# Kernel optimization log

Hardware: AMD Instinct MI355X
Metric: run time of the kernel (lower is better)

Reference implementation:

```python
import jax, jax.numpy as jnp
import numpy as np

B, S, H = 2, 2048, 2048
E, K, HID = 8, 2, 4096          # num_experts, top-k, expert hidden (2*H)
NH, HD = 8, 256                  # attention heads, head_dim
MS, MD = 256, 512                # memory_size, memory_dim
RSTEPS, RD = 3, 512              # reasoning steps, reasoning_dim
SCALE = 16.0                     # sqrt(head_dim)


def setup_inputs() -> dict:
    key = jax.random.key(0)
    ks = iter(jax.random.split(key, 64))
    def w(shape, s=0.02):
        return (jax.random.normal(next(ks), shape, jnp.float32) * s)
    z = lambda *shape: jnp.zeros(shape, jnp.float32)
    inp = {
        'hidden_states': jax.random.normal(next(ks), (B, S, H), jnp.float32),
        'attention_mask': jnp.zeros((B, S), jnp.float32),  # 0 = unmasked (faithful: mask*-1e9 added)
        # MoE
        'gate_w': w((H, E)), 'gate_b': z(E),
        'moe_w1': w((E, H, HID)), 'moe_b1': z(E, HID),
        'moe_w2': w((E, HID, H)), 'moe_b2': z(E, H),
        # memory-augmented attention
        'q_w': w((H, H)), 'q_b': z(H),
        'k_w': w((H, H)), 'k_b': z(H),
        'v_w': w((H, H)), 'v_b': z(H),
        'o_w': w((H, H)), 'o_b': z(H),
        'mem_values': jax.random.normal(next(ks), (MS, MD), jnp.float32),
        'mem_proj_w': w((MD, H)), 'mem_proj_b': z(H),
        'mem_attn_w': w((H, MS)), 'mem_attn_b': z(MS),
        # hierarchical reasoning (stacked over steps)
        'rs_w1': w((RSTEPS, H, RD)), 'rs_b1': z(RSTEPS, RD),
        'rs_w2': w((RSTEPS, RD, H)), 'rs_b2': z(RSTEPS, H),
        'ln_g': jnp.ones((RSTEPS, H), jnp.float32), 'ln_b': z(RSTEPS, H),
        'hg_w1': w((RSTEPS, H, H // 4)), 'hg_b1': z(RSTEPS, H // 4),
        'hg_w2': w((RSTEPS, H // 4, 1)), 'hg_b2': z(RSTEPS, 1),
        'integ_w': w((RSTEPS * H, H)), 'integ_b': z(H),
    }
    return inp


def _layernorm(x, g, b, eps=1e-5):
    m = x.mean(-1, keepdims=True)
    v = ((x - m) ** 2).mean(-1, keepdims=True)
    return (x - m) / jnp.sqrt(v + eps) * g + b


def _forward(hidden_states, attention_mask, gate_w, gate_b, moe_w1, moe_b1, moe_w2, moe_b2,
             q_w, q_b, k_w, k_b, v_w, v_b, o_w, o_b, mem_values, mem_proj_w, mem_proj_b,
             mem_attn_w, mem_attn_b, rs_w1, rs_b1, rs_w2, rs_b2, ln_g, ln_b,
             hg_w1, hg_b1, hg_w2, hg_b2, integ_w, integ_b):
    h = hidden_states
    N = B * S
    # ---- Mixture of Experts (top-k routing, dense combine-weight formulation) ----
    x_flat = h.reshape(N, H)
    gate_probs = jax.nn.softmax(x_flat @ gate_w + gate_b, axis=-1)        # [N,E]
    topk_s, topk_i = jax.lax.top_k(gate_probs, K)                          # [N,K]
    topk_p = jax.nn.softmax(topk_s, axis=-1)                               # renormalize over top-k
    comb = jnp.zeros((N, E), x_flat.dtype).at[jnp.arange(N)[:, None], topk_i].add(topk_p)
    h1 = jax.nn.relu(jnp.einsum('nd,edh->neh', x_flat, moe_w1) + moe_b1)   # [N,E,HID]
    eo = jnp.einsum('neh,ehd->ned', h1, moe_w2) + moe_b2                   # [N,E,H]
    moe_out = jnp.einsum('ned,ne->nd', eo, comb).reshape(B, S, H)
    h = h + 0.5 * moe_out
    # ---- Memory-augmented attention ----
    q = (h @ q_w + q_b).reshape(B, S, NH, HD).transpose(0, 2, 1, 3)
    k = (h @ k_w + k_b).reshape(B, S, NH, HD).transpose(0, 2, 1, 3)
    v = (h @ v_w + v_b).reshape(B, S, NH, HD).transpose(0, 2, 1, 3)
    scores = jnp.einsum('bhqd,bhkd->bhqk', q, k) / SCALE
    scores = scores + attention_mask[:, None, None, :] * (-1e9)
    probs = jax.nn.softmax(scores, axis=-1)
    attn = jnp.einsum('bhqk,bhkd->bhqd', probs, v).transpose(0, 2, 1, 3).reshape(B, S, H)
    mem_p = jax.nn.softmax(h @ mem_attn_w + mem_attn_b, axis=-1)           # [B,S,MS]
    mem_o = (mem_p @ mem_values) @ mem_proj_w + mem_proj_b                 # [B,S,H]
    mem_out = (attn + 0.3 * mem_o) @ o_w + o_b
    h = h + mem_out
    # ---- Hierarchical reasoning ----
    cur = h
    outs = []
    for i in range(RSTEPS):
        so = jax.nn.relu(cur @ rs_w1[i] + rs_b1[i]) @ rs_w2[i] + rs_b2[i]
        so = _layernorm(so, ln_g[i], ln_b[i])
        g = jax.nn.sigmoid(jax.nn.relu(cur @ hg_w1[i] + hg_b1[i]) @ hg_w2[i] + hg_b2[i])  # [B,S,1]
        cur = cur + g * so
        outs.append(cur)
    final = jnp.concatenate(outs, axis=-1) @ integ_w + integ_b
    return h + final


def reference(hidden_states, attention_mask, gate_w, gate_b, moe_w1, moe_b1, moe_w2, moe_b2,
              q_w, q_b, k_w, k_b, v_w, v_b, o_w, o_b, mem_values, mem_proj_w, mem_proj_b,
              mem_attn_w, mem_attn_b, rs_w1, rs_b1, rs_w2, rs_b2, ln_g, ln_b,
              hg_w1, hg_b1, hg_w2, hg_b2, integ_w, integ_b):
    return _forward(hidden_states, attention_mask, gate_w, gate_b, moe_w1, moe_b1, moe_w2, moe_b2,
                    q_w, q_b, k_w, k_b, v_w, v_b, o_w, o_b, mem_values, mem_proj_w, mem_proj_b,
                    mem_attn_w, mem_attn_b, rs_w1, rs_b1, rs_w2, rs_b2, ln_g, ln_b,
                    hg_w1, hg_b1, hg_w2, hg_b2, integ_w, integ_b)
```

## Files before the change

kernel.cpp:

```cpp
#include <hip/hip_runtime.h>
#include <string.h>


typedef __attribute__((ext_vector_type(4))) float f32x4;
typedef __attribute__((ext_vector_type(8))) __bf16 bf16x8;

#define NTOK 4096
#define HDIM 2048
#define AS1 __attribute__((address_space(1)))
#define AS3 __attribute__((address_space(3)))

__device__ __forceinline__ unsigned short f2bf(float f) {
  unsigned u = __float_as_uint(f);
  unsigned r = (u + 0x7fffu + ((u >> 16) & 1u)) >> 16;
  return (unsigned short)r;
}
__device__ __forceinline__ float bf2f(unsigned short u) {
  return __uint_as_float(((unsigned)u) << 16);
}
__device__ __forceinline__ void unpack8(uint4 r, float* v) {
  v[0]=bf2f((unsigned short)(r.x&0xffff)); v[1]=bf2f((unsigned short)(r.x>>16));
  v[2]=bf2f((unsigned short)(r.y&0xffff)); v[3]=bf2f((unsigned short)(r.y>>16));
  v[4]=bf2f((unsigned short)(r.z&0xffff)); v[5]=bf2f((unsigned short)(r.z>>16));
  v[6]=bf2f((unsigned short)(r.w&0xffff)); v[7]=bf2f((unsigned short)(r.w>>16));
}
__device__ __forceinline__ uint4 pack8(const float* v) {
  uint4 r;
  r.x = (unsigned)f2bf(v[0]) | ((unsigned)f2bf(v[1])<<16);
  r.y = (unsigned)f2bf(v[2]) | ((unsigned)f2bf(v[3])<<16);
  r.z = (unsigned)f2bf(v[4]) | ((unsigned)f2bf(v[5])<<16);
  r.w = (unsigned)f2bf(v[6]) | ((unsigned)f2bf(v[7])<<16);
  return r;
}

__global__ void k_tconv(const float* __restrict__ in, unsigned short* __restrict__ out,
                        int R, int C, long inB, long outB) {
  __shared__ float tl[32][33];
  const int z = blockIdx.z;
  const float* ip = in + (long)z * inB;
  unsigned short* op = out + (long)z * outB;
  const int tx = threadIdx.x & 31, ty = threadIdx.x >> 5;
  const int c0 = blockIdx.x * 32, r0 = blockIdx.y * 32;
#pragma unroll
  for (int i = 0; i < 4; i++)
    tl[ty + i*8][tx] = ip[(long)(r0 + ty + i*8) * C + c0 + tx];
  __syncthreads();
#pragma unroll
  for (int i = 0; i < 4; i++)
    op[(long)(c0 + ty + i*8) * R + r0 + tx] = f2bf(tl[tx][ty + i*8]);
}

__global__ void k_tconv4(const float* __restrict__ i0, const float* __restrict__ i1,
                         const float* __restrict__ i2, const float* __restrict__ i3,
                         unsigned short* __restrict__ out) {
  __shared__ float tl[32][33];
  const int z = blockIdx.z;
  const float* ip = (z == 0) ? i0 : (z == 1) ? i1 : (z == 2) ? i2 : i3;
  unsigned short* op = out + ((z < 3) ? (size_t)z * 2048 * 2048 : (size_t)6400 * 2048);
  const int tx = threadIdx.x & 31, ty = threadIdx.x >> 5;
  const int c0 = blockIdx.x * 32, r0 = blockIdx.y * 32;
#pragma unroll
  for (int i = 0; i < 4; i++)
    tl[ty + i*8][tx] = ip[(long)(r0 + ty + i*8) * 2048 + c0 + tx];
  __syncthreads();
#pragma unroll
  for (int i = 0; i < 4; i++)
    op[(long)(c0 + ty + i*8) * 2048 + r0 + tx] = f2bf(tl[tx][ty + i*8]);
}

__global__ void k_tvact(const unsigned short* __restrict__ qkv, unsigned short* __restrict__ vT) {
  __shared__ unsigned short tl[32][33];
  const int z = blockIdx.z, b = z >> 3, hh = z & 7;
  const unsigned short* ip = qkv + (long)b * 2048 * 6400 + 4096 + hh * 256;
  unsigned short* op = vT + (long)z * 256 * 2048;
  const int tx = threadIdx.x & 31, ty = threadIdx.x >> 5;
  const int d0 = blockIdx.x * 32, s0 = blockIdx.y * 32;
#pragma unroll
  for (int i = 0; i < 4; i++)
    tl[ty + i*8][tx] = ip[(long)(s0 + ty + i*8) * 6400 + d0 + tx];
  __syncthreads();
#pragma unroll
  for (int i = 0; i < 4; i++)
    op[(long)(d0 + ty + i*8) * 2048 + s0 + tx] = tl[tx][ty + i*8];
}

__global__ void k_misc(const float* __restrict__ mask, float* __restrict__ mv,
                       const float* __restrict__ qb, const float* __restrict__ kb,
                       const float* __restrict__ vb, const float* __restrict__ mb,
                       float* __restrict__ qkvb,
                       const float* __restrict__ rsb1, const float* __restrict__ hgb1,
                       float* __restrict__ rhb, int* __restrict__ meta) {
  const int b = blockIdx.x, t = threadIdx.x;
  if (b < 16) {
    int i = b * 256 + t; mv[i] = -1e9f * mask[i];
  } else if (b < 41) {
    int i = (b - 16) * 256 + t;
    if (i < 6400)
      qkvb[i] = (i < 2048) ? qb[i] : (i < 4096) ? kb[i - 2048]
              : (i < 6144) ? vb[i - 4096] : mb[i - 6144];
  } else if (b < 47) {
    int i = (b - 41) * 256 + t;
    int s = i >> 9, c = i & 511;
    rhb[s * 1024 + c] = rsb1[i]; rhb[s * 1024 + 512 + c] = hgb1[i];
  } else {
    if (t < 8) meta[t] = 0;
  }
}

__global__ void k_gate(const float* __restrict__ x, const float* __restrict__ gw,
                       const float* __restrict__ gb, int* __restrict__ meta,
                       int* __restrict__ e0a, int* __restrict__ e1a,
                       float* __restrict__ w0a, float* __restrict__ w1a,
                       unsigned short* __restrict__ xb) {
  const int wv = threadIdx.x >> 6, ln = threadIdx.x & 63;
  const int n = blockIdx.x * 4 + wv;
  const float* xr = x + (long)n * HDIM;
  unsigned short* xo = xb + (long)n * HDIM;
  float s[8] = {0,0,0,0,0,0,0,0};
  for (int k = ln; k < HDIM; k += 64) {
    float xv = xr[k];
    xo[k] = f2bf(xv);
    const float* g = gw + (long)k * 8;
#pragma unroll
    for (int e = 0; e < 8; e++) s[e] += xv * g[e];
  }
#pragma unroll
  for (int e = 0; e < 8; e++)
    for (int d = 32; d; d >>= 1) s[e] += __shfl_xor(s[e], d);
  if (ln == 0) {
    float mx = -1e30f;
#pragma unroll
    for (int e = 0; e < 8; e++) { s[e] += gb[e]; mx = fmaxf(mx, s[e]); }
    float p[8], sum = 0.f;
#pragma unroll
    for (int e = 0; e < 8; e++) { p[e] = expf(s[e] - mx); sum += p[e]; }
    float inv = 1.f / sum;
#pragma unroll
    for (int e = 0; e < 8; e++) p[e] *= inv;
    int e0 = 0;
    for (int e = 1; e < 8; e++) if (p[e] > p[e0]) e0 = e;
    int e1 = (e0 == 0) ? 1 : 0;
    for (int e = 0; e < 8; e++) if (e != e0 && p[e] > p[e1]) e1 = e;
    float q = expf(p[e1] - p[e0]);
    float w0 = 1.f / (1.f + q), w1 = q / (1.f + q);
    e0a[n] = e0; e1a[n] = e1; w0a[n] = w0; w1a[n] = w1;
    atomicAdd(&meta[e0], 1); atomicAdd(&meta[e1], 1);
  }
}

__global__ void k_buildmap(int* meta) {
  if (threadIdx.x == 0 && blockIdx.x == 0) {
    int cum = 0, nT = 0;
    for (int e = 0; e < 8; e++) {
      int c = meta[e];
      meta[16 + e] = cum; meta[24 + e] = cum + c; meta[8 + e] = 0;
      int t = (c + 127) >> 7;
      for (int i = 0; i < t; i++) { meta[33 + nT] = e; meta[129 + nT] = cum + i * 128; nT++; }
      cum += c;
    }
    meta[32] = nT;
  }
}

__global__ void k_scatter(int* __restrict__ meta, const int* __restrict__ e0a,
                          const int* __restrict__ e1a, int* __restrict__ s0a,
                          int* __restrict__ s1a, int* __restrict__ srcTok) {
  const int n = blockIdx.x * 256 + threadIdx.x;
  if (n < NTOK) {
    int e0 = e0a[n], e1 = e1a[n];
    int s0 = meta[16 + e0] + atomicAdd(&meta[8 + e0], 1);
    int s1 = meta[16 + e1] + atomicAdd(&meta[8 + e1], 1);
    s0a[n] = s0; s1a[n] = s1; srcTok[s0] = n; srcTok[s1] = n;
  }
}

__global__ void k_combine(const float* __restrict__ h, const unsigned short* __restrict__ eo,
                          const int* __restrict__ s0a, const int* __restrict__ s1a,
                          const float* __restrict__ w0a, const float* __restrict__ w1a,
                          unsigned short* __restrict__ h2b) {
  const int n = blockIdx.x, c = threadIdx.x * 8;
  const float w0 = w0a[n], w1 = w1a[n];
  uint4 a = *(const uint4*)(eo + (long)s0a[n] * HDIM + c);
  uint4 b = *(const uint4*)(eo + (long)s1a[n] * HDIM + c);
  float va[8], vb[8]; unpack8(a, va); unpack8(b, vb);
  const float* hr = h + (long)n * HDIM + c;
  float o[8];
#pragma unroll
  for (int j = 0; j < 8; j++) o[j] = hr[j] + 0.5f * (w0 * va[j] + w1 * vb[j]);
  *(uint4*)(h2b + (long)n * HDIM + c) = pack8(o);
}

__global__ void k_softmax256(const unsigned short* __restrict__ in, long ld,
                             unsigned short* __restrict__ out) {
  const int wv = threadIdx.x >> 6, ln = threadIdx.x & 63;
  const long r = (long)blockIdx.x * 4 + wv;
  uint2 raw = ((const uint2*)(in + r * ld))[ln];
  float v[4];
  v[0]=bf2f((unsigned short)(raw.x&0xffff)); v[1]=bf2f((unsigned short)(raw.x>>16));
  v[2]=bf2f((unsigned short)(raw.y&0xffff)); v[3]=bf2f((unsigned short)(raw.y>>16));
  float m = fmaxf(fmaxf(v[0], v[1]), fmaxf(v[2], v[3]));
  for (int d = 32; d; d >>= 1) m = fmaxf(m, __shfl_xor(m, d));
  float s = 0.f;
#pragma unroll
  for (int j = 0; j < 4; j++) { v[j] = expf(v[j] - m); s += v[j]; }
  for (int d = 32; d; d >>= 1) s += __shfl_xor(s, d);
  const float inv = 1.f / s;
  union { unsigned short u[4]; uint2 d2; } p;
#pragma unroll
  for (int j = 0; j < 4; j++) p.u[j] = f2bf(v[j] * inv);
  ((uint2*)(out + r * 256))[ln] = p.d2;
}

__global__ void k_gdot(const unsigned short* __restrict__ g1, long ld, const float* __restrict__ w,
                       const float* __restrict__ bb, float* __restrict__ gv) {
  const int wv = threadIdx.x >> 6, ln = threadIdx.x & 63;
  const int n = blockIdx.x * 4 + wv;
  uint4 raw = *(const uint4*)(g1 + (long)n * ld + ln * 8);
  float v[8]; unpack8(raw, v);
  const float4 wa = ((const float4*)w)[ln * 2];
  const float4 wb = ((const float4*)w)[ln * 2 + 1];
  float s = v[0]*wa.x + v[1]*wa.y + v[2]*wa.z + v[3]*wa.w
          + v[4]*wb.x + v[5]*wb.y + v[6]*wb.z + v[7]*wb.w;
  for (int d = 32; d; d >>= 1) s += __shfl_xor(s, d);
  if (ln == 0) gv[n] = 1.f / (1.f + expf(-(s + bb[0])));
}

__global__ void k_lnupdate(const unsigned short* __restrict__ so,
                           const unsigned short* __restrict__ curIn,
                           const float* __restrict__ gv, const float* __restrict__ lng,
                           const float* __restrict__ lnb,
                           unsigned short* __restrict__ curbOut,
                           unsigned short* __restrict__ outs, int step) {
  const int n = blockIdx.x, t = threadIdx.x, wv = t >> 6, ln = t & 63, c = t * 8;
  uint4 raw = *(const uint4*)(so + (long)n * 2048 + c);
  float x[8]; unpack8(raw, x);
  float s1 = 0.f, s2 = 0.f;
#pragma unroll
  for (int j = 0; j < 8; j++) { s1 += x[j]; s2 += x[j] * x[j]; }
  for (int d = 32; d; d >>= 1) { s1 += __shfl_xor(s1, d); s2 += __shfl_xor(s2, d); }
  __shared__ float a1[4], a2[4];
  if (ln == 0) { a1[wv] = s1; a2[wv] = s2; }
  __syncthreads();
  s1 = a1[0] + a1[1] + a1[2] + a1[3];
  s2 = a2[0] + a2[1] + a2[2] + a2[3];
  const float mean = s1 * (1.f / 2048.f);
  const float var = s2 * (1.f / 2048.f) - mean * mean;
  const float rstd = rsqrtf(var + 1e-5f);
  const float g = gv[n];
  uint4 ci = *(const uint4*)(curIn + (long)n * 2048 + c);
  float cv[8]; unpack8(ci, cv);
  float o[8];
#pragma unroll
  for (int j = 0; j < 8; j++) {
    float l = (x[j] - mean) * rstd * lng[c + j] + lnb[c + j];
    o[j] = cv[j] + g * l;
  }
  const uint4 pk = pack8(o);
  *(uint4*)(curbOut + (long)n * 2048 + c) = pk;
  *(uint4*)(outs + (long)n * 6144 + (long)step * 2048 + c) = pk;
}

struct GArgs {
  const unsigned short* A; long lda, aSO, aSI;
  const unsigned short* Bt; long ldb, bSO, bSI;
  int M, N, K;
  const float* adv; long advSO, advSI;
  float alpha, rscale;
  const float* rF; long ldrF, rfSO, rfSI;
  const unsigned short* rB; long ldrB, rbSO, rbSI;
  float* oF; long ldoF, ofSO, ofSI;
  unsigned short* oB; long ldoB, obSO, obSI;
  const int* meta;
  const int* srcTok;
};

template <int MOE, int RELU, int RESID, int OUTF, int OUTB>
__global__ __launch_bounds__(512) void gemm_bt(GArgs g) {
  __shared__ unsigned short lds[2 * 16384];
  const int t = threadIdx.x, wv = t >> 6, ln = t & 63, ln15 = ln & 15;
  const int lr8 = ln >> 3;
  const int lsl = (ln & 7) ^ lr8;
  const int bz = blockIdx.z;
  int row0, rowMax;
  const unsigned short *A, *Bt;
  long advO = 0, rFO = 0, rBO = 0, oFO = 0, oBO = 0;
  if constexpr (MOE) {
    const int ty = blockIdx.y;
    if (ty >= g.meta[32]) return;
    const int e = g.meta[33 + ty];
    row0 = g.meta[129 + ty]; rowMax = g.meta[24 + e];
    A = g.A; Bt = g.Bt + (long)e * g.bSO;
    advO = (long)e * g.advSO;
  } else {
    row0 = blockIdx.y << 7; rowMax = g.M;
    const long bo = (long)(bz >> 3), bi = (long)(bz & 7);
    A = g.A + bo * g.aSO + bi * g.aSI;
    Bt = g.Bt + bo * g.bSO + bi * g.bSI;
    advO = bo * g.advSO + bi * g.advSI;
    rFO = bo * g.rfSO + bi * g.rfSI;
    rBO = bo * g.rbSO + bi * g.rbSI;
    oFO = bo * g.ofSO + bi * g.ofSI;
    oBO = bo * g.obSO + bi * g.obSI;
  }
  const int col0 = blockIdx.x << 7;
  const long lda = g.lda, ldb = g.ldb;
  const int wm = (wv >> 2) << 6;
  const int wc = (wv & 3) << 5;

  int grow0, grow1;
  {
    int r0i = row0 + (wv << 4) + lr8;
    int r1i = r0i + 8;
    if constexpr (MOE) {
      r0i = (r0i < rowMax) ? r0i : (rowMax - 1);
      r1i = (r1i < rowMax) ? r1i : (rowMax - 1);
    }
    if constexpr (MOE == 2) { grow0 = g.srcTok[r0i]; grow1 = g.srcTok[r1i]; }
    else { grow0 = r0i; grow1 = r1i; }
  }

  auto STAGE = [&](int kt, unsigned base) {
    const long kk = ((long)kt << 6) + (lsl << 3);
    {
      const int rb = (wv << 4);
      __builtin_amdgcn_global_load_lds(
          (const AS1 void*)(A + (long)grow0 * lda + kk),
          (AS3 void*)(lds + base + (rb << 6)), 16, 0, 0);
      __builtin_amdgcn_global_load_lds(
          (const AS1 void*)(A + (long)grow1 * lda + kk),
          (AS3 void*)(lds + base + ((rb + 8) << 6)), 16, 0, 0);
    }
#pragma unroll
    for (int l = 0; l < 2; ++l) {
      const int rb = (wv << 4) + (l << 3);
      __builtin_amdgcn_global_load_lds(
          (const AS1 void*)(Bt + (long)(col0 + rb + lr8) * ldb + kk),
          (AS3 void*)(lds + base + 8192 + (rb << 6)), 16, 0, 0);
    }
  };

  const f32x4 fz = {0.f, 0.f, 0.f, 0.f};
  f32x4 acc[4][2];
#pragma unroll
  for (int i = 0; i < 4; i++)
#pragma unroll
    for (int j = 0; j < 2; j++) acc[i][j] = fz;

  const int nt = g.K >> 6;

  STAGE(0, 0);
  asm volatile("s_waitcnt vmcnt(0)" ::: "memory");
  __builtin_amdgcn_s_barrier();

  for (int kt = 0; kt < nt; ++kt) {
    const unsigned aB = (kt & 1) ? 16384u : 0u;
    const unsigned nB = aB ^ 16384u;
    if (kt + 1 < nt) STAGE(kt + 1, nB);
#pragma unroll
    for (int ks = 0; ks < 2; ++ks) {
      const int kb = (ks << 2) + (ln >> 4);
      bf16x8 bg[2];
#pragma unroll
      for (int j = 0; j < 2; ++j) {
        const int r = wc + (j << 4) + ln15;
        bg[j] = *(const bf16x8*)(lds + aB + 8192 + (r << 6) + ((kb ^ (r & 7)) << 3));
      }
      __builtin_amdgcn_s_setprio(1);
#pragma unroll
      for (int i = 0; i < 4; ++i) {
        const int r = wm + (i << 4) + ln15;
        bf16x8 a = *(const bf16x8*)(lds + aB + (r << 6) + ((kb ^ (r & 7)) << 3));
#pragma unroll
        for (int j = 0; j < 2; ++j)
          acc[i][j] = __builtin_amdgcn_mfma_f32_16x16x32_bf16(a, bg[j], acc[i][j], 0, 0, 0);
      }
      __builtin_amdgcn_s_setprio(0);
    }
    asm volatile("s_waitcnt vmcnt(0)" ::: "memory");
    __builtin_amdgcn_s_barrier();
  }

#pragma unroll
  for (int i = 0; i < 4; i++) {
#pragma unroll
    for (int j = 0; j < 2; j++) {
      const int cc = col0 + wc + (j << 4) + ln15;
      const float av = g.adv ? g.adv[advO + cc] : 0.f;
#pragma unroll
      for (int r = 0; r < 4; r++) {
        const int rr = row0 + wm + (i << 4) + ((ln >> 4) << 2) + r;
        if (rr < rowMax) {
          float v = g.alpha * acc[i][j][r] + av;
          if constexpr (RELU) v = fmaxf(v, 0.f);
          if constexpr (RESID == 1) v = g.rF[rFO + (long)rr * g.ldrF + cc] + g.rscale * v;
          if constexpr (RESID == 2) v = bf2f(g.rB[rBO + (long)rr * g.ldrB + cc]) + g.rscale * v;
          if constexpr (OUTF) g.oF[oFO + (long)rr * g.ldoF + cc] = v;
          if constexpr (OUTB) g.oB[oBO + (long)rr * g.ldoB + cc] = f2bf(v);
        }
      }
    }
  }
}

__global__ __launch_bounds__(512) void k_fa(const unsigned short* __restrict__ qkvm,
                                            const unsigned short* __restrict__ Vt,
                                            const float* __restrict__ msk,
                                            unsigned short* __restrict__ O) {
  __shared__ unsigned short sm[34816];
  __shared__ float msk_s[2048];
  __shared__ float m_run[64], l_run[64], fac[64], mnv[64], tsm[128], tss[128];
  const int t = threadIdx.x, wv = t >> 6, ln = t & 63, ln15 = ln & 15;
  const int rt = blockIdx.x, bh = blockIdx.y;
  const int b = bh >> 3, hh = bh & 7;
  const int q0 = rt << 6;
  const unsigned short* Bq = qkvm + (long)b * 2048 * 6400;

#pragma unroll
  for (int l = 0; l < 4; ++l) {
    const int li = l * 512 + t;
    const int p = li >> 9, r = (li >> 3) & 63, s = li & 7;
    __builtin_amdgcn_global_load_lds(
        (const AS1 void*)(Bq + (long)(q0 + r) * 6400 + hh * 256 + p * 64 + ((s ^ (r & 7)) << 3)),
        (AS3 void*)(sm + li * 8), 16, 0, 0);
  }
#pragma unroll
  for (int l = 0; l < 4; ++l) {
    const int i = l * 512 + t;
    msk_s[i] = msk[b * 2048 + i];
  }
  if (t < 64) { m_run[t] = -3.0e38f; l_run[t] = 0.f; }

  auto STAGEKV = [&](int kt) {
#pragma unroll
    for (int l = 0; l < 2; ++l) {
      const int li = l * 512 + t;
      const int p = li >> 8, r = (li >> 3) & 31, s = li & 7;
      __builtin_amdgcn_global_load_lds(
          (const AS1 void*)(Bq + (long)(kt * 32 + r) * 6400 + 2048 + hh * 256 + p * 64 + ((s ^ (r & 7)) << 3)),
          (AS3 void*)(sm + 16384 + li * 8), 16, 0, 0);
    }
#pragma unroll
    for (int l = 0; l < 2; ++l) {
      const int li = l * 512 + t;
      const int r = li >> 2, s = li & 3;
      __builtin_amdgcn_global_load_lds(
          (const AS1 void*)(Vt + (long)bh * 524288 + (long)r * 2048 + kt * 32 + ((s ^ ((r >> 1) & 3)) << 3)),
          (AS3 void*)(sm + 24576 + li * 8), 16, 0, 0);
    }
  };
  STAGEKV(0);
  asm volatile("s_waitcnt vmcnt(0)" ::: "memory");
  __syncthreads();

  const int rw = wv >> 1, cw = wv & 1;
  const int wc = wv << 5;
  const int rowbase = (rw << 4) + ((ln >> 4) << 2);
  const f32x4 fz = {0.f, 0.f, 0.f, 0.f};
  f32x4 acc[4][2];
#pragma unroll
  for (int i = 0; i < 4; i++)
#pragma unroll
    for (int j = 0; j < 2; j++) acc[i][j] = fz;

  for (int kt = 0; kt < 64; ++kt) {
    f32x4 sAcc = fz;
#pragma unroll
    for (int ks = 0; ks < 8; ++ks) {
      const int kp = ks >> 1;
      const int kb = ((ks & 1) << 2) + (ln >> 4);
      const int ra = (rw << 4) + ln15;
      bf16x8 a = *(const bf16x8*)(sm + kp * 4096 + (ra << 6) + ((kb ^ (ra & 7)) << 3));
      const int rb = (cw << 4) + ln15;
      bf16x8 bb = *(const bf16x8*)(sm + 16384 + kp * 2048 + (rb << 6) + ((kb ^ (rb & 7)) << 3));
      sAcc = __builtin_amdgcn_mfma_f32_16x16x32_bf16(a, bb, sAcc, 0, 0, 0);
    }
    float sv[4];
    const float mk = msk_s[(kt << 5) + (cw << 4) + ln15];
#pragma unroll
    for (int r = 0; r < 4; ++r) {
      sv[r] = sAcc[r] * 0.0625f + mk;
      float mr = sv[r];
#pragma unroll
      for (int d = 1; d < 16; d <<= 1) mr = fmaxf(mr, __shfl_xor(mr, d));
      if (ln15 == 0) tsm[((rowbase + r) << 1) + cw] = mr;
    }
    __syncthreads();
    if (t < 64) {
      if (kt > 0) l_run[t] = l_run[t] * fac[t] + tss[t << 1] + tss[(t << 1) + 1];
      const float mt = fmaxf(tsm[t << 1], tsm[(t << 1) + 1]);
      const float mn = fmaxf(m_run[t], mt);
      fac[t] = expf(m_run[t] - mn);
      mnv[t] = mn; m_run[t] = mn;
    }
    __syncthreads();
#pragma unroll
    for (int r = 0; r < 4; ++r) {
      const int row = rowbase + r;
      const float p = expf(sv[r] - mnv[row]);
      const int col = (cw << 4) + ln15;
      sm[32768 + (row << 5) + (((col >> 3) ^ ((row >> 1) & 3)) << 3) + (col & 7)] = f2bf(p);
      float sr = p;
#pragma unroll
      for (int d = 1; d < 16; d <<= 1) sr += __shfl_xor(sr, d);
      if (ln15 == 0) tss[(row << 1) + cw] = sr;
    }
#pragma unroll
    for (int i = 0; i < 4; ++i) {
      const int rw2 = (i << 4) + ((ln >> 4) << 2);
#pragma unroll
      for (int r = 0; r < 4; ++r) {
        const float fv = fac[rw2 + r];
        acc[i][0][r] *= fv; acc[i][1][r] *= fv;
      }
    }
    __syncthreads();
    const int kb2 = ln >> 4;
#pragma unroll
    for (int i = 0; i < 4; ++i) {
      const int ra = (i << 4) + ln15;
      bf16x8 a = *(const bf16x8*)(sm + 32768 + (ra << 5) + ((kb2 ^ ((ra >> 1) & 3)) << 3));
#pragma unroll
      for (int j = 0; j < 2; ++j) {
        const int rv = wc + (j << 4) + ln15;
        bf16x8 bv = *(const bf16x8*)(sm + 24576 + (rv << 5) + ((kb2 ^ ((rv >> 1) & 3)) << 3));
        acc[i][j] = __builtin_amdgcn_mfma_f32_16x16x32_bf16(a, bv, acc[i][j], 0, 0, 0);
      }
    }
    __syncthreads();
    if (kt + 1 < 64) STAGEKV(kt + 1);
    asm volatile("s_waitcnt vmcnt(0)" ::: "memory");
    __syncthreads();
  }
  if (t < 64) {
    const float l = l_run[t] * fac[t] + tss[t << 1] + tss[(t << 1) + 1];
    fac[t] = 1.f / l;
  }
  __syncthreads();
  unsigned short* Ob = O + (long)b * 2048 * 2048 + hh * 256;
#pragma unroll
  for (int i = 0; i < 4; ++i) {
#pragma unroll
    for (int j = 0; j < 2; ++j) {
      const int cc = wc + (j << 4) + ln15;
#pragma unroll
      for (int r = 0; r < 4; ++r) {
        const int row = (i << 4) + ((ln >> 4) << 2) + r;
        Ob[(long)(q0 + row) * 2048 + cc] = f2bf(acc[i][j][r] * fac[row]);
      }
    }
  }
}

static constexpr size_t O_W1T = 0;
static constexpr size_t O_W2T = O_W1T + (size_t)8 * 4096 * 2048 * 2;
static constexpr size_t O_QT  = O_W2T + (size_t)8 * 4096 * 2048 * 2;
static constexpr size_t O_OT  = O_QT + (size_t)6400 * 2048 * 2;
static constexpr size_t O_MPT = O_QT + (size_t)8448 * 2048 * 2;
static constexpr size_t O_MVT = O_MPT + (size_t)2048 * 512 * 2;
static constexpr size_t O_RH1 = O_MVT + (size_t)512 * 256 * 2;
static constexpr size_t O_RS2 = O_RH1 + (size_t)3 * 1024 * 2048 * 2;
static constexpr size_t O_IGT = O_RS2 + (size_t)3 * 2048 * 512 * 2;
static constexpr size_t O_META= O_IGT + (size_t)2048 * 6144 * 2;
static constexpr size_t O_E0  = O_META + 4096;
static constexpr size_t O_E1  = O_E0 + 16384;
static constexpr size_t O_W0  = O_E1 + 16384;
static constexpr size_t O_W1  = O_W0 + 16384;
static constexpr size_t O_S0  = O_W1 + 16384;
static constexpr size_t O_S1  = O_S0 + 16384;
static constexpr size_t O_SRC = O_S1 + 16384;
static constexpr size_t O_MSK = O_SRC + 32768;
static constexpr size_t O_GV  = O_MSK + 16384;
static constexpr size_t O_QKVB= O_GV + 16384;
static constexpr size_t O_RHB = O_QKVB + 6400 * 4;
static constexpr size_t O_H2B = O_RHB + 3072 * 4;
static constexpr size_t O_H3B = O_H2B + (size_t)4096 * 2048 * 2;
static constexpr size_t O_ATT = O_H3B + (size_t)4096 * 2048 * 2;
static constexpr size_t O_AO2 = O_ATT + (size_t)4096 * 2048 * 2;
static constexpr size_t O_MPB = O_AO2 + (size_t)4096 * 2048 * 2;
static constexpr size_t O_MPV = O_MPB + (size_t)4096 * 256 * 2;
static constexpr size_t O_AR  = O_MPV + (size_t)4096 * 512 * 2;
static constexpr size_t O_XB = O_AR;
static constexpr size_t O_H1 = O_XB + (size_t)4096 * 2048 * 2 + (size_t)8192 * 2048 * 2;
static constexpr size_t O_EO = O_H1 + (size_t)8192 * 4096 * 2;
static constexpr size_t O_QB = O_XB + (size_t)4096 * 2048 * 2;
static constexpr size_t O_VT = O_QB + (size_t)4096 * 6400 * 2;
static constexpr size_t O_T1 = O_QB;
static constexpr size_t O_SOB= O_T1 + (size_t)4096 * 1024 * 2;
static constexpr size_t O_CRB= O_SOB + (size_t)4096 * 2048 * 2;
static constexpr size_t O_OUS= O_CRB + (size_t)4096 * 2048 * 2;

extern "C" void kernel_launch(void* const* d_in, const int* in_sizes, int n_in,
                              void* d_out, int out_size, void* d_ws, size_t ws_size,
                              hipStream_t stream) {
  (void)in_sizes; (void)n_in; (void)out_size; (void)ws_size;
  const float* h        = (const float*)d_in[0];
  const float* mask     = (const float*)d_in[1];
  const float* gate_w   = (const float*)d_in[2];
  const float* gate_b   = (const float*)d_in[3];
  const float* moe_w1   = (const float*)d_in[4];
  const float* moe_b1   = (const float*)d_in[5];
  const float* moe_w2   = (const float*)d_in[6];
  const float* moe_b2   = (const float*)d_in[7];
  const float* q_w      = (const float*)d_in[8];
  const float* q_b      = (const float*)d_in[9];
  const float* k_w      = (const float*)d_in[10];
  const float* k_b      = (const float*)d_in[11];
  const float* v_w      = (const float*)d_in[12];
  const float* v_b      = (const float*)d_in[13];
  const float* o_w      = (const float*)d_in[14];
  const float* o_b      = (const float*)d_in[15];
  const float* mem_vals = (const float*)d_in[16];
  const float* mproj_w  = (const float*)d_in[17];
  const float* mproj_b  = (const float*)d_in[18];
  const float* mattn_w  = (const float*)d_in[19];
  const float* mattn_b  = (const float*)d_in[20];
  const float* rs_w1    = (const float*)d_in[21];
  const float* rs_b1    = (const float*)d_in[22];
  const float* rs_w2    = (const float*)d_in[23];
  const float* rs_b2    = (const float*)d_in[24];
  const float* ln_g     = (const float*)d_in[25];
  const float* ln_b     = (const float*)d_in[26];
  const float* hg_w1    = (const float*)d_in[27];
  const float* hg_b1    = (const float*)d_in[28];
  const float* hg_w2    = (const float*)d_in[29];
  const float* hg_b2    = (const float*)d_in[30];
  const float* integ_w  = (const float*)d_in[31];
  const float* integ_b  = (const float*)d_in[32];

  char* ws = (char*)d_ws;
  auto U = [&](size_t o) { return (unsigned short*)(ws + o); };
  auto F = [&](size_t o) { return (float*)(ws + o); };
  auto I = [&](size_t o) { return (int*)(ws + o); };

  k_tconv<<<dim3(128, 64, 8), 256, 0, stream>>>(moe_w1, U(O_W1T), 2048, 4096, 8388608, 8388608);
  k_tconv<<<dim3(64, 128, 8), 256, 0, stream>>>(moe_w2, U(O_W2T), 4096, 2048, 8388608, 8388608);
  k_tconv4<<<dim3(64, 64, 4), 256, 0, stream>>>(q_w, k_w, v_w, o_w, U(O_QT));
  k_tconv<<<dim3(8, 64, 1), 256, 0, stream>>>(mattn_w, U(O_QT) + (size_t)6144 * 2048, 2048, 256, 0, 0);
  k_tconv<<<dim3(64, 16, 1), 256, 0, stream>>>(mproj_w, U(O_MPT), 512, 2048, 0, 0);
  k_tconv<<<dim3(16, 8, 1), 256, 0, stream>>>(mem_vals, U(O_MVT), 256, 512, 0, 0);
  k_tconv<<<dim3(16, 64, 3), 256, 0, stream>>>(rs_w1, U(O_RH1), 2048, 512, 2048 * 512, 1024 * 2048);
  k_tconv<<<dim3(16, 64, 3), 256, 0, stream>>>(hg_w1, U(O_RH1) + (size_t)512 * 2048, 2048, 512,
                                               2048 * 512, 1024 * 2048);
  k_tconv<<<dim3(64, 16, 3), 256, 0, stream>>>(rs_w2, U(O_RS2), 512, 2048, 512 * 2048, 512 * 2048);
  k_tconv<<<dim3(64, 192, 1), 256, 0, stream>>>(integ_w, U(O_IGT), 6144, 2048, 0, 0);
  k_misc<<<48, 256, 0, stream>>>(mask, F(O_MSK), q_b, k_b, v_b, mattn_b, F(O_QKVB),
                                 rs_b1, hg_b1, F(O_RHB), I(O_META));

  k_gate<<<1024, 256, 0, stream>>>(h, gate_w, gate_b, I(O_META), I(O_E0), I(O_E1),
                                   F(O_W0), F(O_W1), U(O_XB));
  k_buildmap<<<1, 1, 0, stream>>>(I(O_META));
  k_scatter<<<16, 256, 0, stream>>>(I(O_META), I(O_E0), I(O_E1), I(O_S0), I(O_S1), I(O_SRC));

  GArgs z0; memset(&z0, 0, sizeof(z0)); z0.alpha = 1.f; z0.rscale = 1.f;
  {
    GArgs g = z0;
    g.A = U(O_XB); g.lda = 2048;
    g.Bt = U(O_W1T); g.ldb = 2048; g.bSO = (long)4096 * 2048;
    g.N = 4096; g.K = 2048;
    g.adv = moe_b1; g.advSO = 4096;
    g.oB = U(O_H1); g.ldoB = 4096;
    g.meta = I(O_META); g.srcTok = I(O_SRC);
    gemm_bt<2, 1, 0, 0, 1><<<dim3(32, 72, 1), 512, 0, stream>>>(g);
  }
  {
    GArgs g = z0;
    g.A = U(O_H1); g.lda = 4096;
    g.Bt = U(O_W2T); g.ldb = 4096; g.bSO = (long)2048 * 4096;
    g.N = 2048; g.K = 4096;
    g.adv = moe_b2; g.advSO = 2048;
    g.oB = U(O_EO); g.ldoB = 2048;
    g.meta = I(O_META);
    gemm_bt<1, 0, 0, 0, 1><<<dim3(16, 72, 1), 512, 0, stream>>>(g);
  }
  k_combine<<<4096, 256, 0, stream>>>(h, U(O_EO), I(O_S0), I(O_S1), F(O_W0), F(O_W1), U(O_H2B));

  {
    GArgs g = z0;
    g.A = U(O_H2B); g.lda = 2048; g.M = 4096; g.N = 6400; g.K = 2048;
    g.Bt = U(O_QT); g.ldb = 2048;
    g.adv = F(O_QKVB);
    g.oB = U(O_QB); g.ldoB = 6400;
    gemm_bt<0, 0, 0, 0, 1><<<dim3(50, 32, 1), 512, 0, stream>>>(g);
  }
  k_tvact<<<dim3(8, 64, 16), 256, 0, stream>>>(U(O_QB), U(O_VT));
  k_fa<<<dim3(32, 16, 1), 512, 0, stream>>>(U(O_QB), U(O_VT), F(O_MSK), U(O_ATT));
  k_softmax256<<<1024, 256, 0, stream>>>(U(O_QB) + 6144, 6400, U(O_MPB));
  {
    GArgs g = z0;
    g.A = U(O_MPB); g.lda = 256; g.Bt = U(O_MVT); g.ldb = 256;
    g.M = 4096; g.N = 512; g.K = 256;
    g.oB = U(O_MPV); g.ldoB = 512;
    gemm_bt<0, 0, 0, 0, 1><<<dim3(4, 32, 1), 512, 0, stream>>>(g);
  }
  {
    GArgs g = z0;
    g.A = U(O_MPV); g.lda = 512; g.Bt = U(O_MPT); g.ldb = 512;
    g.M = 4096; g.N = 2048; g.K = 512;
    g.adv = mproj_b;
    g.rB = U(O_ATT); g.ldrB = 2048; g.rscale = 0.3f;
    g.oB = U(O_AO2); g.ldoB = 2048;
    gemm_bt<0, 0, 2, 0, 1><<<dim3(16, 32, 1), 512, 0, stream>>>(g);
  }
  {
    GArgs g = z0;
    g.A = U(O_AO2); g.lda = 2048; g.Bt = U(O_OT); g.ldb = 2048;
    g.M = 4096; g.N = 2048; g.K = 2048;
    g.adv = o_b;
    g.rB = U(O_H2B); g.ldrB = 2048; g.rscale = 1.f;
    g.oB = U(O_H3B); g.ldoB = 2048;
    gemm_bt<0, 0, 2, 0, 1><<<dim3(16, 32, 1), 512, 0, stream>>>(g);
  }

  for (int i = 0; i < 3; i++) {
    const unsigned short* curb = (i == 0) ? U(O_H3B) : U(O_CRB);
    {
      GArgs g = z0;
      g.A = curb; g.lda = 2048;
      g.Bt = U(O_RH1) + (size_t)i * 1024 * 2048; g.ldb = 2048;
      g.M = 4096; g.N = 1024; g.K = 2048;
      g.adv = F(O_RHB) + i * 1024;
      g.oB = U(O_T1); g.ldoB = 1024;
      gemm_bt<0, 1, 0, 0, 1><<<dim3(8, 32, 1), 512, 0, stream>>>(g);
    }
    {
      GArgs g = z0;
      g.A = U(O_T1); g.lda = 1024;
      g.Bt = U(O_RS2) + (size_t)i * 2048 * 512; g.ldb = 512;
      g.M = 4096; g.N = 2048; g.K = 512;
      g.adv = rs_b2 + i * 2048;
      g.oB = U(O_SOB); g.ldoB = 2048;
      gemm_bt<0, 0, 0, 0, 1><<<dim3(16, 32, 1), 512, 0, stream>>>(g);
    }
    k_gdot<<<1024, 256, 0, stream>>>(U(O_T1) + 512, 1024, hg_w2 + i * 512, hg_b2 + i, F(O_GV));
    k_lnupdate<<<4096, 256, 0, stream>>>(U(O_SOB), curb, F(O_GV), ln_g + i * 2048,
                                         ln_b + i * 2048, U(O_CRB), U(O_OUS), i);
  }
  {
    GArgs g = z0;
    g.A = U(O_OUS); g.lda = 6144; g.Bt = U(O_IGT); g.ldb = 6144;
    g.M = 4096; g.N = 2048; g.K = 6144;
    g.adv = integ_b;
    g.rB = U(O_H3B); g.ldrB = 2048; g.rscale = 1.f;
    g.oF = (float*)d_out; g.ldoF = 2048;
    gemm_bt<0, 0, 2, 1, 0><<<dim3(16, 32, 1), 512, 0, stream>>>(g);
  }
}
```

Measured before the change: 1.626 ms.

## Keep Q in registers and double-buffer K/V tiles in flash attention

Q fragments are loaded once into registers instead of being staged in LDS, which frees LDS for a second K/V buffer. The next K/V tile is then prefetched into the alternate buffer at the start of each iteration, so the global-to-LDS copy overlaps the QK and PV MFMAs, and one barrier per iteration is removed. The QK dot product is split across two accumulators to shorten the MFMA dependency chain. In exchange it uses more registers (eight bf16x8 Q vectors per thread), which may lower occupancy.

```diff
diff --git a/kernel.cpp b/kernel.cpp
--- a/kernel.cpp
+++ b/kernel.cpp
@@ -415,14 +415,16 @@
   const int q0 = rt << 6;
   const unsigned short* Bq = qkvm + (long)b * 2048 * 6400;
 
-#pragma unroll
-  for (int l = 0; l < 4; ++l) {
-    const int li = l * 512 + t;
-    const int p = li >> 9, r = (li >> 3) & 63, s = li & 7;
-    __builtin_amdgcn_global_load_lds(
-        (const AS1 void*)(Bq + (long)(q0 + r) * 6400 + hh * 256 + p * 64 + ((s ^ (r & 7)) << 3)),
-        (AS3 void*)(sm + li * 8), 16, 0, 0);
-  }
+  const int rw = wv >> 1, cw = wv & 1;
+  const int wc = wv << 5;
+  const int rowbase = (rw << 4) + ((ln >> 4) << 2);
+  const int ra = (rw << 4) + ln15;
+
+  bf16x8 qreg[8];
+#pragma unroll
+  for (int ks = 0; ks < 8; ++ks)
+    qreg[ks] = *(const bf16x8*)(Bq + (long)(q0 + ra) * 6400 + hh * 256 + ks * 32 + ((ln >> 4) << 3));
+
 #pragma unroll
   for (int l = 0; l < 4; ++l) {
     const int i = l * 512 + t;
@@ -430,14 +432,14 @@
   }
   if (t < 64) { m_run[t] = -3.0e38f; l_run[t] = 0.f; }
 
-  auto STAGEKV = [&](int kt) {
+  auto STAGEKV = [&](int kt, int buf) {
 #pragma unroll
     for (int l = 0; l < 2; ++l) {
       const int li = l * 512 + t;
       const int p = li >> 8, r = (li >> 3) & 31, s = li & 7;
       __builtin_amdgcn_global_load_lds(
           (const AS1 void*)(Bq + (long)(kt * 32 + r) * 6400 + 2048 + hh * 256 + p * 64 + ((s ^ (r & 7)) << 3)),
-          (AS3 void*)(sm + 16384 + li * 8), 16, 0, 0);
+          (AS3 void*)(sm + buf * 8192 + li * 8), 16, 0, 0);
     }
 #pragma unroll
     for (int l = 0; l < 2; ++l) {
@@ -445,16 +447,13 @@
       const int r = li >> 2, s = li & 3;
       __builtin_amdgcn_global_load_lds(
           (const AS1 void*)(Vt + (long)bh * 524288 + (long)r * 2048 + kt * 32 + ((s ^ ((r >> 1) & 3)) << 3)),
-          (AS3 void*)(sm + 24576 + li * 8), 16, 0, 0);
+          (AS3 void*)(sm + 16384 + buf * 8192 + li * 8), 16, 0, 0);
     }
   };
-  STAGEKV(0);
+  STAGEKV(0, 0);
   asm volatile("s_waitcnt vmcnt(0)" ::: "memory");
   __syncthreads();
 
-  const int rw = wv >> 1, cw = wv & 1;
-  const int wc = wv << 5;
-  const int rowbase = (rw << 4) + ((ln >> 4) << 2);
   const f32x4 fz = {0.f, 0.f, 0.f, 0.f};
   f32x4 acc[4][2];
 #pragma unroll
@@ -463,22 +462,23 @@
     for (int j = 0; j < 2; j++) acc[i][j] = fz;
 
   for (int kt = 0; kt < 64; ++kt) {
-    f32x4 sAcc = fz;
+    const int cur = kt & 1;
+    if (kt + 1 < 64) STAGEKV(kt + 1, cur ^ 1);
+    f32x4 sA = fz, sB = fz;
 #pragma unroll
     for (int ks = 0; ks < 8; ++ks) {
       const int kp = ks >> 1;
       const int kb = ((ks & 1) << 2) + (ln >> 4);
-      const int ra = (rw << 4) + ln15;
-      bf16x8 a = *(const bf16x8*)(sm + kp * 4096 + (ra << 6) + ((kb ^ (ra & 7)) << 3));
       const int rb = (cw << 4) + ln15;
-      bf16x8 bb = *(const bf16x8*)(sm + 16384 + kp * 2048 + (rb << 6) + ((kb ^ (rb & 7)) << 3));
-      sAcc = __builtin_amdgcn_mfma_f32_16x16x32_bf16(a, bb, sAcc, 0, 0, 0);
+      bf16x8 bb = *(const bf16x8*)(sm + cur * 8192 + kp * 2048 + (rb << 6) + ((kb ^ (rb & 7)) << 3));
+      if (ks & 1) sB = __builtin_amdgcn_mfma_f32_16x16x32_bf16(qreg[ks], bb, sB, 0, 0, 0);
+      else        sA = __builtin_amdgcn_mfma_f32_16x16x32_bf16(qreg[ks], bb, sA, 0, 0, 0);
     }
     float sv[4];
     const float mk = msk_s[(kt << 5) + (cw << 4) + ln15];
 #pragma unroll
     for (int r = 0; r < 4; ++r) {
-      sv[r] = sAcc[r] * 0.0625f + mk;
+      sv[r] = (sA[r] + sB[r]) * 0.0625f + mk;
       float mr = sv[r];
 #pragma unroll
       for (int d = 1; d < 16; d <<= 1) mr = fmaxf(mr, __shfl_xor(mr, d));
@@ -517,17 +517,15 @@
     const int kb2 = ln >> 4;
 #pragma unroll
     for (int i = 0; i < 4; ++i) {
-      const int ra = (i << 4) + ln15;
-      bf16x8 a = *(const bf16x8*)(sm + 32768 + (ra << 5) + ((kb2 ^ ((ra >> 1) & 3)) << 3));
+      const int rp = (i << 4) + ln15;
+      bf16x8 a = *(const bf16x8*)(sm + 32768 + (rp << 5) + ((kb2 ^ ((rp >> 1) & 3)) << 3));
 #pragma unroll
       for (int j = 0; j < 2; ++j) {
         const int rv = wc + (j << 4) + ln15;
-        bf16x8 bv = *(const bf16x8*)(sm + 24576 + (rv << 5) + ((kb2 ^ ((rv >> 1) & 3)) << 3));
+        bf16x8 bv = *(const bf16x8*)(sm + 16384 + cur * 8192 + (rv << 5) + ((kb2 ^ ((rv >> 1) & 3)) << 3));
         acc[i][j] = __builtin_amdgcn_mfma_f32_16x16x32_bf16(a, bv, acc[i][j], 0, 0, 0);
       }
     }
-    __syncthreads();
-    if (kt + 1 < 64) STAGEKV(kt + 1);
     asm volatile("s_waitcnt vmcnt(0)" ::: "memory");
     __syncthreads();
   }
```

New measurement: 1.746 ms. +7.4%, slower.
